# Kernel tuning notes

Measured on AMD Instinct MI355X. Metric: run time of the kernel, lower is better.

## Reference

```python
import jax, jax.numpy as jnp
import numpy as np

B, S, E, H, D = 2, 2048, 512, 8, 64
NEG = -1e10


def setup_inputs() -> dict:
    key = jax.random.key(0)
    k1, k2, k3, k4, k5, k6 = jax.random.split(key, 6)
    inputs = jax.random.normal(k1, (B, S, E), dtype=jnp.float32)
    keys = jax.random.normal(k2, (B, S, H, D), dtype=jnp.float32)
    values = jax.random.normal(k3, (B, S, H, D), dtype=jnp.float32)
    # xavier-uniform style scale for square weights
    lim = float(np.sqrt(6.0 / (E + H * D)))
    query_weights = jax.random.uniform(k4, (E, H * D), minval=-lim, maxval=lim, dtype=jnp.float32)
    output_weights = jax.random.uniform(k5, (H * D, E), minval=-lim, maxval=lim, dtype=jnp.float32)
    mask = jax.random.randint(k6, (B, S, S), 0, 2).astype(jnp.bool_)
    return {"inputs": inputs, "keys": keys, "values": values,
            "query_weights": query_weights, "output_weights": output_weights,
            "mask": mask}


def reference(inputs, keys, values, query_weights, output_weights, mask):
    # project queries: (B,S,E) @ (E,H*D) -> (B,S,H,D)
    q = jnp.matmul(inputs, query_weights).reshape(B, S, H, D)
    # scores: (B,H,Sq,Sk)
    scores = jnp.einsum('bqhd,bkhd->bhqk', q, keys) / jnp.sqrt(jnp.float32(D))
    # masked_fill(mask, -1e10); mask broadcasts over heads
    scores = jnp.where(mask[:, None, :, :], jnp.float32(NEG), scores)
    probs = jax.nn.softmax(scores, axis=-1)
    # (B,H,Sq,Sk) x (B,Sk,H,D) -> (B,Sq,H,D)
    out = jnp.einsum('bhqk,bkhd->bqhd', probs, values)
    out = out.reshape(B, S, H * D)
    return jnp.matmul(out, output_weights)
```

## Files before the change

kernel.cpp:

```cpp
#include <hip/hip_runtime.h>
#include <hip/hip_bf16.h>

namespace {

constexpr int B = 2, S = 2048, E = 512, H = 8, D = 64, HD = 512;
constexpr float NEG = -1e10f;
constexpr float SCALE = 0.125f;
constexpr int LDK = 72;
constexpr int LDV = 136;
constexpr int PLD = 40;

typedef __attribute__((ext_vector_type(8))) short bf16x8;
typedef __attribute__((ext_vector_type(4))) unsigned short u16x4;
typedef __attribute__((ext_vector_type(4))) float f32x4;
typedef __attribute__((ext_vector_type(4))) float float4v;

__device__ __forceinline__ ushort f2b(float x) {
  __hip_bfloat16 h = __float2bfloat16(x);
  return *reinterpret_cast<const ushort*>(&h);
}
__device__ __forceinline__ float b2f_u(ushort u) {
  __hip_bfloat16 h = *reinterpret_cast<const __hip_bfloat16*>(&u);
  return __bfloat162float(h);
}

__global__ __launch_bounds__(256) void prep_kv_kernel(
    const float* __restrict__ K, const float* __restrict__ V,
    ushort* __restrict__ Kbf, ushort* __restrict__ Vtbf) {
  __shared__ ushort Vn[64][76];
  const int bid = blockIdx.x;
  const int kt = bid & 31;
  const int bh = bid >> 5;
  const int b = bh >> 3, h = bh & 7;
  const int k0 = kt * 64;
  const int t = threadIdx.x;
#pragma unroll
  for (int i = 0; i < 4; ++i) {
    int c = i * 256 + t;
    int kk = c >> 4, d4 = (c & 15) * 4;
    size_t g = ((size_t)(b * 2048 + k0 + kk) * 8 + h) * 64 + d4;
    float4v kv = *(const float4v*)(K + g);
    float4v vv = *(const float4v*)(V + g);
    u16x4 kp = {f2b(kv.x), f2b(kv.y), f2b(kv.z), f2b(kv.w)};
    u16x4 vp = {f2b(vv.x), f2b(vv.y), f2b(vv.z), f2b(vv.w)};
    *(u16x4*)(Kbf + ((size_t)(bh * 2048 + k0 + kk)) * 64 + d4) = kp;
    *(u16x4*)&Vn[kk][d4] = vp;
  }
  __syncthreads();
#pragma unroll
  for (int i = 0; i < 2; ++i) {
    int c = i * 256 + t;
    int kc8 = (c & 7) * 8, d = c >> 3;
    union { ushort u[8]; bf16x8 v; } p;
#pragma unroll
    for (int j = 0; j < 8; ++j) p.u[j] = Vn[kc8 + j][d];
    *(bf16x8*)(Vtbf + ((size_t)(bh * 64 + d)) * 2048 + k0 + kc8) = p.v;
  }
}

__global__ __launch_bounds__(256) void proj_q_kernel(
    const float* __restrict__ A, const float* __restrict__ Wg, ushort* __restrict__ Qbf) {
  __shared__ __align__(16) ushort As_hi[64][PLD];
  __shared__ __align__(16) ushort As_lo[64][PLD];
  __shared__ __align__(16) ushort Ws[64][PLD];

  const int tid = threadIdx.x;
  const int lane = tid & 63;
  const int w = tid >> 6;
  const int col = lane & 15;
  const int quad = lane >> 4;
  const int m0 = blockIdx.y * 64;
  const int n0 = blockIdx.x * 64;
  const int wm = (w & 1) * 32;
  const int wn = (w >> 1) * 32;
  const int ar = tid >> 2;
  const int ak = (tid & 3) * 8;
  const int wn_s = tid & 63;
  const int wk_s = tid >> 6;

  f32x4 acc[2][2];
#pragma unroll
  for (int i = 0; i < 2; ++i)
#pragma unroll
    for (int j = 0; j < 2; ++j) acc[i][j] = f32x4{0.f, 0.f, 0.f, 0.f};

  for (int kt = 0; kt < 16; ++kt) {
    const int k0 = kt * 32;
    {
      const float* Ap = A + (size_t)(m0 + ar) * 512 + k0 + ak;
      float4v v0 = *(const float4v*)Ap;
      float4v v1 = *(const float4v*)(Ap + 4);
      float a[8] = {v0.x, v0.y, v0.z, v0.w, v1.x, v1.y, v1.z, v1.w};
      union { ushort u[8]; bf16x8 v; } hi, lo;
#pragma unroll
      for (int j = 0; j < 8; ++j) {
        ushort hh = f2b(a[j]);
        hi.u[j] = hh;
        lo.u[j] = f2b(a[j] - b2f_u(hh));
      }
      *(bf16x8*)&As_hi[ar][ak] = hi.v;
      *(bf16x8*)&As_lo[ar][ak] = lo.v;
    }
#pragma unroll
    for (int p = 0; p < 8; ++p) {
      int k = p * 4 + wk_s;
      Ws[wn_s][k] = f2b(Wg[(size_t)(k0 + k) * 512 + n0 + wn_s]);
    }
    __syncthreads();

    bf16x8 ah[2], al[2], wb[2];
#pragma unroll
    for (int i = 0; i < 2; ++i) {
      ah[i] = *(const bf16x8*)&As_hi[wm + i * 16 + col][quad * 8];
      al[i] = *(const bf16x8*)&As_lo[wm + i * 16 + col][quad * 8];
    }
#pragma unroll
    for (int j = 0; j < 2; ++j)
      wb[j] = *(const bf16x8*)&Ws[wn + j * 16 + col][quad * 8];
#pragma unroll
    for (int i = 0; i < 2; ++i)
#pragma unroll
      for (int j = 0; j < 2; ++j) {
        acc[i][j] = __builtin_amdgcn_mfma_f32_16x16x32_bf16(ah[i], wb[j], acc[i][j], 0, 0, 0);
        acc[i][j] = __builtin_amdgcn_mfma_f32_16x16x32_bf16(al[i], wb[j], acc[i][j], 0, 0, 0);
      }
    __syncthreads();
  }

#pragma unroll
  for (int i = 0; i < 2; ++i)
#pragma unroll
    for (int j = 0; j < 2; ++j)
#pragma unroll
      for (int r = 0; r < 4; ++r) {
        int m = m0 + wm + i * 16 + quad * 4 + r;
        int n = n0 + wn + j * 16 + col;
        int b = m >> 11, q = m & 2047, h = n >> 6, dd = n & 63;
        Qbf[((size_t)(b * 8 + h) * 2048 + q) * 64 + dd] = f2b(acc[i][j][r]);
      }
}

__global__ __launch_bounds__(256) void proj_out_kernel(
    const ushort* __restrict__ A, const float* __restrict__ Wg, float* __restrict__ C) {
  __shared__ __align__(16) ushort As[64][PLD];
  __shared__ __align__(16) ushort Ws[64][PLD];

  const int tid = threadIdx.x;
  const int lane = tid & 63;
  const int w = tid >> 6;
  const int col = lane & 15;
  const int quad = lane >> 4;
  const int m0 = blockIdx.y * 64;
  const int n0 = blockIdx.x * 64;
  const int wm = (w & 1) * 32;
  const int wn = (w >> 1) * 32;
  const int ar = tid >> 2;
  const int ak = (tid & 3) * 8;
  const int wn_s = tid & 63;
  const int wk_s = tid >> 6;

  f32x4 acc[2][2];
#pragma unroll
  for (int i = 0; i < 2; ++i)
#pragma unroll
    for (int j = 0; j < 2; ++j) acc[i][j] = f32x4{0.f, 0.f, 0.f, 0.f};

  for (int kt = 0; kt < 16; ++kt) {
    const int k0 = kt * 32;
    *(bf16x8*)&As[ar][ak] = *(const bf16x8*)(A + (size_t)(m0 + ar) * 512 + k0 + ak);
#pragma unroll
    for (int p = 0; p < 8; ++p) {
      int k = p * 4 + wk_s;
      Ws[wn_s][k] = f2b(Wg[(size_t)(k0 + k) * 512 + n0 + wn_s]);
    }
    __syncthreads();

    bf16x8 ah[2], wb[2];
#pragma unroll
    for (int i = 0; i < 2; ++i)
      ah[i] = *(const bf16x8*)&As[wm + i * 16 + col][quad * 8];
#pragma unroll
    for (int j = 0; j < 2; ++j)
      wb[j] = *(const bf16x8*)&Ws[wn + j * 16 + col][quad * 8];
#pragma unroll
    for (int i = 0; i < 2; ++i)
#pragma unroll
      for (int j = 0; j < 2; ++j)
        acc[i][j] = __builtin_amdgcn_mfma_f32_16x16x32_bf16(ah[i], wb[j], acc[i][j], 0, 0, 0);
    __syncthreads();
  }

#pragma unroll
  for (int i = 0; i < 2; ++i)
#pragma unroll
    for (int j = 0; j < 2; ++j)
#pragma unroll
      for (int r = 0; r < 4; ++r)
        C[(size_t)(m0 + wm + i * 16 + quad * 4 + r) * 512 + n0 + wn + j * 16 + col] =
            acc[i][j][r];
}

__global__ __launch_bounds__(256) void flash_attn_kernel(
    const ushort* __restrict__ Qbf, const ushort* __restrict__ Kbf,
    const ushort* __restrict__ Vtbf, const int* __restrict__ mask,
    ushort* __restrict__ Op) {
  __shared__ __align__(16) ushort Qs[64][LDK];
  __shared__ __align__(16) ushort Ks[128][LDK];
  __shared__ __align__(16) ushort Vt[64][LDV];
  __shared__ __align__(16) ushort Ps[64][LDV];

  const int bid = blockIdx.x;
  const int qt = bid & 31;
  const int bh = bid >> 5;
  const int b = bh >> 3, h = bh & 7;
  const int q0 = qt * 64;
  const int tid = threadIdx.x;
  const int lane = tid & 63;
  const int w = tid >> 6;
  const int col = lane & 15;
  const int quad = lane >> 4;

  const ushort* Qt = Qbf + (size_t)(bh * 2048 + q0) * 64;
#pragma unroll
  for (int i = 0; i < 2; ++i) {
    int c = i * 256 + tid;
    *(bf16x8*)&Qs[c >> 3][(c & 7) * 8] = *(const bf16x8*)(Qt + c * 8);
  }
  __syncthreads();

  f32x4 oacc[4];
  float m[4], l[4];
#pragma unroll
  for (int c = 0; c < 4; ++c) oacc[c] = f32x4{0.f, 0.f, 0.f, 0.f};
#pragma unroll
  for (int r = 0; r < 4; ++r) { m[r] = -INFINITY; l[r] = 0.f; }

  const bf16x8 a0 = *(const bf16x8*)&Qs[w * 16 + col][quad * 8];
  const bf16x8 a1 = *(const bf16x8*)&Qs[w * 16 + col][32 + quad * 8];

  for (int kt = 0; kt < 16; ++kt) {
    const int k0 = kt * 128;
    const ushort* Ktile = Kbf + (size_t)(bh * 2048 + k0) * 64;
    const ushort* Vtile = Vtbf + (size_t)(bh * 64) * 2048 + k0;
#pragma unroll
    for (int i = 0; i < 4; ++i) {
      int c = i * 256 + tid;
      *(bf16x8*)&Ks[c >> 3][(c & 7) * 8] = *(const bf16x8*)(Ktile + c * 8);
      int d = c >> 4, k8 = (c & 15) * 8;
      *(bf16x8*)&Vt[d][k8] = *(const bf16x8*)(Vtile + (size_t)d * 2048 + k8);
    }
    __syncthreads();

    int mk[4][8];
    {
      const int* mp = mask + (size_t)(b * S + q0 + w * 16 + quad * 4) * S + k0 + col;
#pragma unroll
      for (int r = 0; r < 4; ++r)
#pragma unroll
        for (int c = 0; c < 8; ++c) mk[r][c] = mp[(size_t)r * S + c * 16];
    }

    f32x4 sc[8];
#pragma unroll
    for (int c = 0; c < 8; ++c) sc[c] = f32x4{0.f, 0.f, 0.f, 0.f};
#pragma unroll
    for (int c = 0; c < 8; ++c) {
      bf16x8 kb0 = *(const bf16x8*)&Ks[c * 16 + col][quad * 8];
      bf16x8 kb1 = *(const bf16x8*)&Ks[c * 16 + col][32 + quad * 8];
      sc[c] = __builtin_amdgcn_mfma_f32_16x16x32_bf16(a0, kb0, sc[c], 0, 0, 0);
      sc[c] = __builtin_amdgcn_mfma_f32_16x16x32_bf16(a1, kb1, sc[c], 0, 0, 0);
    }

    float tmax[4] = {-INFINITY, -INFINITY, -INFINITY, -INFINITY};
#pragma unroll
    for (int c = 0; c < 8; ++c)
#pragma unroll
      for (int r = 0; r < 4; ++r) {
        float s = mk[r][c] ? NEG : sc[c][r] * SCALE;
        sc[c][r] = s;
        tmax[r] = fmaxf(tmax[r], s);
      }
#pragma unroll
    for (int r = 0; r < 4; ++r)
#pragma unroll
      for (int off = 1; off < 16; off <<= 1)
        tmax[r] = fmaxf(tmax[r], __shfl_xor(tmax[r], off));

    float al[4], rs[4];
#pragma unroll
    for (int r = 0; r < 4; ++r) {
      float mn = fmaxf(m[r], tmax[r]);
      al[r] = __expf(m[r] - mn);
      m[r] = mn;
      rs[r] = 0.f;
    }
#pragma unroll
    for (int c = 0; c < 8; ++c)
#pragma unroll
      for (int r = 0; r < 4; ++r) {
        float p = __expf(sc[c][r] - m[r]);
        sc[c][r] = p;
        rs[r] += p;
      }
#pragma unroll
    for (int r = 0; r < 4; ++r) {
#pragma unroll
      for (int off = 1; off < 16; off <<= 1) rs[r] += __shfl_xor(rs[r], off);
      l[r] = l[r] * al[r] + rs[r];
    }
#pragma unroll
    for (int c = 0; c < 4; ++c)
#pragma unroll
      for (int r = 0; r < 4; ++r) oacc[c][r] *= al[r];

#pragma unroll
    for (int r = 0; r < 4; ++r)
#pragma unroll
      for (int c = 0; c < 8; ++c)
        Ps[w * 16 + quad * 4 + r][c * 16 + col] = f2b(sc[c][r]);
    __threadfence_block();

    bf16x8 pa[4];
#pragma unroll
    for (int kb = 0; kb < 4; ++kb)
      pa[kb] = *(const bf16x8*)&Ps[w * 16 + col][kb * 32 + quad * 8];
#pragma unroll
    for (int c = 0; c < 4; ++c)
#pragma unroll
      for (int kb = 0; kb < 4; ++kb) {
        bf16x8 vb = *(const bf16x8*)&Vt[c * 16 + col][kb * 32 + quad * 8];
        oacc[c] = __builtin_amdgcn_mfma_f32_16x16x32_bf16(pa[kb], vb, oacc[c], 0, 0, 0);
      }
    __syncthreads();
  }

  float inv[4];
#pragma unroll
  for (int r = 0; r < 4; ++r) inv[r] = 1.f / l[r];
#pragma unroll
  for (int c = 0; c < 4; ++c)
#pragma unroll
    for (int r = 0; r < 4; ++r)
      Op[(size_t)(b * S + q0 + w * 16 + quad * 4 + r) * HD + h * D + c * 16 + col] =
          f2b(oacc[c][r] * inv[r]);
}

}

extern "C" void kernel_launch(void* const* d_in, const int* in_sizes, int n_in,
                              void* d_out, int out_size, void* d_ws, size_t ws_size,
                              hipStream_t stream) {
  const float* inputs = (const float*)d_in[0];
  const float* keys   = (const float*)d_in[1];
  const float* values = (const float*)d_in[2];
  const float* wq     = (const float*)d_in[3];
  const float* wo     = (const float*)d_in[4];
  const int*   maskp  = (const int*)d_in[5];
  float* out = (float*)d_out;

  ushort* Qbf   = (ushort*)d_ws;
  ushort* Kbf   = Qbf + (size_t)2097152;
  ushort* Vtbf  = Kbf + (size_t)2097152;
  ushort* attnb = Vtbf + (size_t)2097152;

  dim3 blk(256);
  proj_q_kernel<<<dim3(8, 64), blk, 0, stream>>>(inputs, wq, Qbf);
  prep_kv_kernel<<<dim3(512), blk, 0, stream>>>(keys, values, Kbf, Vtbf);
  flash_attn_kernel<<<dim3(512), blk, 0, stream>>>(Qbf, Kbf, Vtbf, maskp, attnb);
  proj_out_kernel<<<dim3(8, 64), blk, 0, stream>>>(attnb, wo, out);
}
```

Before: 193.8 us.

## Bit-pack mask, pre-transpose weights, and restructure attention softmax per lane-row

After: 202.6 us. 4.5% more time.

```diff
diff --git a/kernel.cpp b/kernel.cpp
--- a/kernel.cpp
+++ b/kernel.cpp
@@ -4,10 +4,8 @@
 namespace {
 
 constexpr int B = 2, S = 2048, E = 512, H = 8, D = 64, HD = 512;
-constexpr float NEG = -1e10f;
 constexpr float SCALE = 0.125f;
-constexpr int LDK = 72;
-constexpr int LDV = 136;
+constexpr float SL = 0.125f * 1.44269504f;
 constexpr int PLD = 40;
 
 typedef __attribute__((ext_vector_type(8))) short bf16x8;
@@ -27,7 +25,7 @@
 __global__ __launch_bounds__(256) void prep_kv_kernel(
     const float* __restrict__ K, const float* __restrict__ V,
     ushort* __restrict__ Kbf, ushort* __restrict__ Vtbf) {
-  __shared__ ushort Vn[64][76];
+  __shared__ __align__(16) ushort Vn[64][76];
   const int bid = blockIdx.x;
   const int kt = bid & 31;
   const int bh = bid >> 5;
@@ -58,8 +56,53 @@
   }
 }
 
+__global__ __launch_bounds__(256) void prep_mask_kernel(
+    const int* __restrict__ m, uint* __restrict__ keep) {
+  int gid = blockIdx.x * 256 + threadIdx.x;
+  int row = gid >> 6, j = gid & 63;
+  const int4* p = (const int4*)(m + (size_t)row * 2048 + j * 32);
+  uint w = 0;
+#pragma unroll
+  for (int q = 0; q < 8; ++q) {
+    int4 v = p[q];
+    w |= (uint)(v.x == 0) << (q * 4 + 0);
+    w |= (uint)(v.y == 0) << (q * 4 + 1);
+    w |= (uint)(v.z == 0) << (q * 4 + 2);
+    w |= (uint)(v.w == 0) << (q * 4 + 3);
+  }
+  keep[gid] = w;
+}
+
+__global__ __launch_bounds__(256) void prep_wt_kernel(
+    const float* __restrict__ Wq, const float* __restrict__ Wo,
+    ushort* __restrict__ Wtq, ushort* __restrict__ Wto) {
+  __shared__ __align__(16) ushort T[64][68];
+  const float* Wsrc = blockIdx.y ? Wo : Wq;
+  ushort* Wdst = blockIdx.y ? Wto : Wtq;
+  const int k0 = (blockIdx.x & 7) * 64, n0 = (blockIdx.x >> 3) * 64;
+  const int t = threadIdx.x;
+#pragma unroll
+  for (int i = 0; i < 4; ++i) {
+    int c = i * 256 + t;
+    int kk = c >> 4, n4 = (c & 15) * 4;
+    float4v v = *(const float4v*)(Wsrc + (size_t)(k0 + kk) * 512 + n0 + n4);
+    u16x4 p = {f2b(v.x), f2b(v.y), f2b(v.z), f2b(v.w)};
+    *(u16x4*)&T[kk][n4] = p;
+  }
+  __syncthreads();
+#pragma unroll
+  for (int i = 0; i < 2; ++i) {
+    int c = i * 256 + t;
+    int n = c >> 3, k8 = (c & 7) * 8;
+    union { ushort u[8]; bf16x8 v; } p;
+#pragma unroll
+    for (int j = 0; j < 8; ++j) p.u[j] = T[k8 + j][n];
+    *(bf16x8*)(Wdst + (size_t)(n0 + n) * 512 + k0 + k8) = p.v;
+  }
+}
+
 __global__ __launch_bounds__(256) void proj_q_kernel(
-    const float* __restrict__ A, const float* __restrict__ Wg, ushort* __restrict__ Qbf) {
+    const float* __restrict__ A, const ushort* __restrict__ Wt, ushort* __restrict__ Qbf) {
   __shared__ __align__(16) ushort As_hi[64][PLD];
   __shared__ __align__(16) ushort As_lo[64][PLD];
   __shared__ __align__(16) ushort Ws[64][PLD];
@@ -75,8 +118,8 @@
   const int wn = (w >> 1) * 32;
   const int ar = tid >> 2;
   const int ak = (tid & 3) * 8;
-  const int wn_s = tid & 63;
-  const int wk_s = tid >> 6;
+  const int wn2 = tid >> 2;
+  const int wkc = (tid & 3) * 8;
 
   f32x4 acc[2][2];
 #pragma unroll
@@ -101,11 +144,7 @@
       *(bf16x8*)&As_hi[ar][ak] = hi.v;
       *(bf16x8*)&As_lo[ar][ak] = lo.v;
     }
-#pragma unroll
-    for (int p = 0; p < 8; ++p) {
-      int k = p * 4 + wk_s;
-      Ws[wn_s][k] = f2b(Wg[(size_t)(k0 + k) * 512 + n0 + wn_s]);
-    }
+    *(bf16x8*)&Ws[wn2][wkc] = *(const bf16x8*)(Wt + (size_t)(n0 + wn2) * 512 + k0 + wkc);
     __syncthreads();
 
     bf16x8 ah[2], al[2], wb[2];
@@ -141,7 +180,7 @@
 }
 
 __global__ __launch_bounds__(256) void proj_out_kernel(
-    const ushort* __restrict__ A, const float* __restrict__ Wg, float* __restrict__ C) {
+    const ushort* __restrict__ A, const ushort* __restrict__ Wt, float* __restrict__ C) {
   __shared__ __align__(16) ushort As[64][PLD];
   __shared__ __align__(16) ushort Ws[64][PLD];
 
@@ -156,8 +195,8 @@
   const int wn = (w >> 1) * 32;
   const int ar = tid >> 2;
   const int ak = (tid & 3) * 8;
-  const int wn_s = tid & 63;
-  const int wk_s = tid >> 6;
+  const int wn2 = tid >> 2;
+  const int wkc = (tid & 3) * 8;
 
   f32x4 acc[2][2];
 #pragma unroll
@@ -168,11 +207,7 @@
   for (int kt = 0; kt < 16; ++kt) {
     const int k0 = kt * 32;
     *(bf16x8*)&As[ar][ak] = *(const bf16x8*)(A + (size_t)(m0 + ar) * 512 + k0 + ak);
-#pragma unroll
-    for (int p = 0; p < 8; ++p) {
-      int k = p * 4 + wk_s;
-      Ws[wn_s][k] = f2b(Wg[(size_t)(k0 + k) * 512 + n0 + wn_s]);
-    }
+    *(bf16x8*)&Ws[wn2][wkc] = *(const bf16x8*)(Wt + (size_t)(n0 + wn2) * 512 + k0 + wkc);
     __syncthreads();
 
     bf16x8 ah[2], wb[2];
@@ -202,12 +237,11 @@
 
 __global__ __launch_bounds__(256) void flash_attn_kernel(
     const ushort* __restrict__ Qbf, const ushort* __restrict__ Kbf,
-    const ushort* __restrict__ Vtbf, const int* __restrict__ mask,
+    const ushort* __restrict__ Vtbf, const uint* __restrict__ keep,
     ushort* __restrict__ Op) {
-  __shared__ __align__(16) ushort Qs[64][LDK];
-  __shared__ __align__(16) ushort Ks[128][LDK];
-  __shared__ __align__(16) ushort Vt[64][LDV];
-  __shared__ __align__(16) ushort Ps[64][LDV];
+  __shared__ __align__(16) ushort Ks[128][72];
+  __shared__ __align__(16) ushort Vt[64][136];
+  __shared__ __align__(16) ushort PQ[64][136];
 
   const int bid = blockIdx.x;
   const int qt = bid & 31;
@@ -219,24 +253,24 @@
   const int w = tid >> 6;
   const int col = lane & 15;
   const int quad = lane >> 4;
+  const int quad4 = quad * 4;
 
   const ushort* Qt = Qbf + (size_t)(bh * 2048 + q0) * 64;
 #pragma unroll
   for (int i = 0; i < 2; ++i) {
     int c = i * 256 + tid;
-    *(bf16x8*)&Qs[c >> 3][(c & 7) * 8] = *(const bf16x8*)(Qt + c * 8);
+    *(bf16x8*)&PQ[c >> 3][(c & 7) * 8] = *(const bf16x8*)(Qt + c * 8);
   }
   __syncthreads();
+  const bf16x8 qb0 = *(const bf16x8*)&PQ[w * 16 + col][quad * 8];
+  const bf16x8 qb1 = *(const bf16x8*)&PQ[w * 16 + col][32 + quad * 8];
 
   f32x4 oacc[4];
-  float m[4], l[4];
 #pragma unroll
   for (int c = 0; c < 4; ++c) oacc[c] = f32x4{0.f, 0.f, 0.f, 0.f};
-#pragma unroll
-  for (int r = 0; r < 4; ++r) { m[r] = -INFINITY; l[r] = 0.f; }
-
-  const bf16x8 a0 = *(const bf16x8*)&Qs[w * 16 + col][quad * 8];
-  const bf16x8 a1 = *(const bf16x8*)&Qs[w * 16 + col][32 + quad * 8];
+  float m = -INFINITY, l = 0.f;
+
+  const uint4* kr = (const uint4*)keep + ((size_t)(b * 2048 + q0 + w * 16 + col)) * 16;
 
   for (int kt = 0; kt < 16; ++kt) {
     const int k0 = kt * 128;
@@ -251,79 +285,68 @@
     }
     __syncthreads();
 
-    int mk[4][8];
-    {
-      const int* mp = mask + (size_t)(b * S + q0 + w * 16 + quad * 4) * S + k0 + col;
-#pragma unroll
-      for (int r = 0; r < 4; ++r)
-#pragma unroll
-        for (int c = 0; c < 8; ++c) mk[r][c] = mp[(size_t)r * S + c * 16];
-    }
+    const uint4 mw = kr[kt];
+    const uint mwords[4] = {mw.x, mw.y, mw.z, mw.w};
 
     f32x4 sc[8];
 #pragma unroll
-    for (int c = 0; c < 8; ++c) sc[c] = f32x4{0.f, 0.f, 0.f, 0.f};
-#pragma unroll
-    for (int c = 0; c < 8; ++c) {
-      bf16x8 kb0 = *(const bf16x8*)&Ks[c * 16 + col][quad * 8];
-      bf16x8 kb1 = *(const bf16x8*)&Ks[c * 16 + col][32 + quad * 8];
-      sc[c] = __builtin_amdgcn_mfma_f32_16x16x32_bf16(a0, kb0, sc[c], 0, 0, 0);
-      sc[c] = __builtin_amdgcn_mfma_f32_16x16x32_bf16(a1, kb1, sc[c], 0, 0, 0);
-    }
-
-    float tmax[4] = {-INFINITY, -INFINITY, -INFINITY, -INFINITY};
-#pragma unroll
-    for (int c = 0; c < 8; ++c)
+    for (int t = 0; t < 8; ++t) sc[t] = f32x4{0.f, 0.f, 0.f, 0.f};
+#pragma unroll
+    for (int t = 0; t < 8; ++t) {
+      bf16x8 ka0 = *(const bf16x8*)&Ks[t * 16 + col][quad * 8];
+      bf16x8 ka1 = *(const bf16x8*)&Ks[t * 16 + col][32 + quad * 8];
+      sc[t] = __builtin_amdgcn_mfma_f32_16x16x32_bf16(ka0, qb0, sc[t], 0, 0, 0);
+      sc[t] = __builtin_amdgcn_mfma_f32_16x16x32_bf16(ka1, qb1, sc[t], 0, 0, 0);
+    }
+
+    float mx = -INFINITY;
+#pragma unroll
+    for (int t = 0; t < 8; ++t)
+#pragma unroll
+      for (int r = 0; r < 4; ++r) mx = fmaxf(mx, sc[t][r]);
+    mx *= SL;
+    mx = fmaxf(mx, __shfl_xor(mx, 16));
+    mx = fmaxf(mx, __shfl_xor(mx, 32));
+
+    const float mn = fmaxf(m, mx);
+    const float alpha = exp2f(m - mn);
+    m = mn;
+
+    float rs = 0.f;
+#pragma unroll
+    for (int t = 0; t < 8; ++t) {
+      uint sh = mwords[t >> 1] >> ((t & 1) * 16 + quad4);
 #pragma unroll
       for (int r = 0; r < 4; ++r) {
-        float s = mk[r][c] ? NEG : sc[c][r] * SCALE;
-        sc[c][r] = s;
-        tmax[r] = fmaxf(tmax[r], s);
+        float p = exp2f(fmaf(sc[t][r], SL, -mn));
+        p = ((sh >> r) & 1u) ? p : 0.f;
+        sc[t][r] = p;
+        rs += p;
       }
-#pragma unroll
-    for (int r = 0; r < 4; ++r)
-#pragma unroll
-      for (int off = 1; off < 16; off <<= 1)
-        tmax[r] = fmaxf(tmax[r], __shfl_xor(tmax[r], off));
-
-    float al[4], rs[4];
-#pragma unroll
-    for (int r = 0; r < 4; ++r) {
-      float mn = fmaxf(m[r], tmax[r]);
-      al[r] = __expf(m[r] - mn);
-      m[r] = mn;
-      rs[r] = 0.f;
-    }
-#pragma unroll
-    for (int c = 0; c < 8; ++c)
-#pragma unroll
-      for (int r = 0; r < 4; ++r) {
-        float p = __expf(sc[c][r] - m[r]);
-        sc[c][r] = p;
-        rs[r] += p;
-      }
-#pragma unroll
-    for (int r = 0; r < 4; ++r) {
-#pragma unroll
-      for (int off = 1; off < 16; off <<= 1) rs[r] += __shfl_xor(rs[r], off);
-      l[r] = l[r] * al[r] + rs[r];
-    }
+    }
+    rs += __shfl_xor(rs, 16);
+    rs += __shfl_xor(rs, 32);
+    l = l * alpha + rs;
+
+    float alO[4];
+#pragma unroll
+    for (int r = 0; r < 4; ++r) alO[r] = __shfl(alpha, quad4 + r);
 #pragma unroll
     for (int c = 0; c < 4; ++c)
 #pragma unroll
-      for (int r = 0; r < 4; ++r) oacc[c][r] *= al[r];
-
-#pragma unroll
-    for (int r = 0; r < 4; ++r)
-#pragma unroll
-      for (int c = 0; c < 8; ++c)
-        Ps[w * 16 + quad * 4 + r][c * 16 + col] = f2b(sc[c][r]);
+      for (int r = 0; r < 4; ++r) oacc[c][r] *= alO[r];
+
+#pragma unroll
+    for (int t = 0; t < 8; ++t) {
+      u16x4 pk = {f2b(sc[t][0]), f2b(sc[t][1]), f2b(sc[t][2]), f2b(sc[t][3])};
+      *(u16x4*)&PQ[w * 16 + col][t * 16 + quad4] = pk;
+    }
     __threadfence_block();
 
     bf16x8 pa[4];
 #pragma unroll
     for (int kb = 0; kb < 4; ++kb)
-      pa[kb] = *(const bf16x8*)&Ps[w * 16 + col][kb * 32 + quad * 8];
+      pa[kb] = *(const bf16x8*)&PQ[w * 16 + col][kb * 32 + quad * 8];
 #pragma unroll
     for (int c = 0; c < 4; ++c)
 #pragma unroll
@@ -334,15 +357,16 @@
     __syncthreads();
   }
 
-  float inv[4];
-#pragma unroll
-  for (int r = 0; r < 4; ++r) inv[r] = 1.f / l[r];
+  const float inv = 1.f / l;
+  float invO[4];
+#pragma unroll
+  for (int r = 0; r < 4; ++r) invO[r] = __shfl(inv, quad4 + r);
 #pragma unroll
   for (int c = 0; c < 4; ++c)
 #pragma unroll
     for (int r = 0; r < 4; ++r)
-      Op[(size_t)(b * S + q0 + w * 16 + quad * 4 + r) * HD + h * D + c * 16 + col] =
-          f2b(oacc[c][r] * inv[r]);
+      Op[(size_t)(b * S + q0 + w * 16 + quad4 + r) * HD + h * D + c * 16 + col] =
+          f2b(oacc[c][r] * invO[r]);
 }
 
 }
@@ -358,14 +382,21 @@
   const int*   maskp  = (const int*)d_in[5];
   float* out = (float*)d_out;
 
-  ushort* Qbf   = (ushort*)d_ws;
-  ushort* Kbf   = Qbf + (size_t)2097152;
-  ushort* Vtbf  = Kbf + (size_t)2097152;
-  ushort* attnb = Vtbf + (size_t)2097152;
+  ushort* Kbf  = (ushort*)d_out;
+  ushort* Vtbf = Kbf + (size_t)2097152;
+
+  char* ws = (char*)d_ws;
+  ushort* Qbf   = (ushort*)ws;
+  ushort* attnb = (ushort*)(ws + (4 << 20));
+  uint*   keep  = (uint*)(ws + (8 << 20));
+  ushort* Wtq   = (ushort*)(ws + (9 << 20));
+  ushort* Wto   = (ushort*)(ws + (9 << 20) + (512 << 10));
 
   dim3 blk(256);
-  proj_q_kernel<<<dim3(8, 64), blk, 0, stream>>>(inputs, wq, Qbf);
+  prep_wt_kernel<<<dim3(64, 2), blk, 0, stream>>>(wq, wo, Wtq, Wto);
   prep_kv_kernel<<<dim3(512), blk, 0, stream>>>(keys, values, Kbf, Vtbf);
-  flash_attn_kernel<<<dim3(512), blk, 0, stream>>>(Qbf, Kbf, Vtbf, maskp, attnb);
-  proj_out_kernel<<<dim3(8, 64), blk, 0, stream>>>(attnb, wo, out);
-}
+  prep_mask_kernel<<<dim3(1024), blk, 0, stream>>>(maskp, keep);
+  proj_q_kernel<<<dim3(8, 64), blk, 0, stream>>>(inputs, Wtq, Qbf);
+  flash_attn_kernel<<<dim3(512), blk, 0, stream>>>(Qbf, Kbf, Vtbf, keep, attnb);
+  proj_out_kernel<<<dim3(8, 64), blk, 0, stream>>>(attnb, Wto, out);
+}
```
